# Kernel tuning notes

Hardware: AMD Instinct MI355X
Metric: run time of the kernel (lower is better)

Reference implementation:

```python
import jax, jax.numpy as jnp
import numpy as np

IN_FEATURES = 4096
OUT_FEATURES = 4096
GROUP_SIZE = 128


def _unpack_int4_last_dim(packed):
    # packed: [..., P] int32 -> [..., P*8] int32 nibbles in [0,15]
    shifts = jnp.arange(0, 32, 4, dtype=jnp.int32)
    u = (packed[..., None] >> shifts) & 15
    return u.reshape(*packed.shape[:-1], packed.shape[-1] * 8)


def setup_inputs() -> dict:
    key = jax.random.key(0)
    k1, k2, k3, k4, k5 = jax.random.split(key, 5)
    groups = IN_FEATURES // GROUP_SIZE  # 32
    x = jax.random.normal(k1, (4096, IN_FEATURES), dtype=jnp.float32)
    qweight = jax.random.randint(k2, (OUT_FEATURES, IN_FEATURES // 8), 0, 2147483647, dtype=jnp.int32)
    qzeros = jax.random.randint(k3, (OUT_FEATURES, groups // 8), 0, 2147483647, dtype=jnp.int32)
    scales = jax.random.uniform(k4, (OUT_FEATURES, groups), dtype=jnp.float32) * 0.02 + 0.001
    bias = jax.random.normal(k5, (OUT_FEATURES,), dtype=jnp.float32)
    return {"x": x, "qweight": qweight, "qzeros": qzeros, "scales": scales, "bias": bias}


def _dequantize_weight(qweight, qzeros, scales):
    # qweight: [out, in/8] -> w_int: [out, in]
    w_int = _unpack_int4_last_dim(qweight).astype(jnp.float32)
    # qzeros: [out, groups/8] -> zeros: [out, groups]
    zeros = _unpack_int4_last_dim(qzeros).astype(jnp.float32)
    group_ids = jnp.arange(IN_FEATURES) // GROUP_SIZE  # [in]
    # expand per-group scale/zero along in_features
    w = (w_int - zeros[:, group_ids]) * scales[:, group_ids]  # [out, in]
    return w


def reference(x, qweight, qzeros, scales, bias):
    w = _dequantize_weight(qweight, qzeros, scales)  # [out, in] fp32
    return x @ w.T + bias  # [tokens, out]
```

## Files before the change

### kernel.cpp

```cpp
#include <hip/hip_runtime.h>
#include <hip/hip_bf16.h>

#define TOKENS 4096
#define IN_F   4096
#define OUT_F  4096

typedef __bf16 bf16x8 __attribute__((ext_vector_type(8)));
typedef float  f32x4  __attribute__((ext_vector_type(4)));
typedef unsigned int u32;
typedef u32 u32x4 __attribute__((ext_vector_type(4)));

#define DEQ_BLOCKS 2048
#define CVT_BLOCKS 4096

__device__ __forceinline__ void gld_lds16(const void* g, void* l) {
    __builtin_amdgcn_global_load_lds(
        (const __attribute__((address_space(1))) u32*)g,
        (__attribute__((address_space(3))) u32*)l,
        16, 0, 0);
}

__global__ __launch_bounds__(256) void prep_kernel(
        const u32* __restrict__ qweight, const u32* __restrict__ qzeros,
        const float* __restrict__ scales, const float* __restrict__ x,
        __bf16* __restrict__ W, __bf16* __restrict__ A) {
    const int tid = threadIdx.x;
    if (blockIdx.x < DEQ_BLOCKS) {
        int idx4 = blockIdx.x * 256 + tid;
        int n  = idx4 >> 7;
        int p4 = (idx4 & 127) << 2;
        int g  = p4 >> 4;
        u32 qz = qzeros[(n << 2) + (g >> 3)];
        float z = (float)((qz >> ((g & 7) * 4)) & 15);
        float s = scales[(n << 5) + g];
        u32x4 qw = *(const u32x4*)(qweight + (size_t)n * 512 + p4);
        __bf16* dst = W + (size_t)n * IN_F + p4 * 8;
#pragma unroll
        for (int c = 0; c < 4; ++c) {
            bf16x8 h;
#pragma unroll
            for (int j = 0; j < 8; ++j) {
                float w = ((float)((qw[c] >> (4 * j)) & 15) - z) * s;
                h[j] = (__bf16)w;
            }
            *(bf16x8*)(dst + c * 8) = h;
        }
    } else {
        int idx = (blockIdx.x - DEQ_BLOCKS) * 256 + tid;
        const f32x4* xp = (const f32x4*)x + (size_t)idx * 4;
        f32x4 v0 = xp[0], v1 = xp[1], v2 = xp[2], v3 = xp[3];
        bf16x8 h0, h1;
#pragma unroll
        for (int j = 0; j < 4; ++j) {
            h0[j] = (__bf16)v0[j]; h0[4 + j] = (__bf16)v1[j];
            h1[j] = (__bf16)v2[j]; h1[4 + j] = (__bf16)v3[j];
        }
        bf16x8* ap = (bf16x8*)A + (size_t)idx * 2;
        ap[0] = h0; ap[1] = h1;
    }
}

__global__ __launch_bounds__(512, 2) void gemm8p(
        const __bf16* __restrict__ A, const __bf16* __restrict__ B,
        const float* __restrict__ bias, float* __restrict__ C) {
    __shared__ __align__(16) char lsA[65536];
    __shared__ __align__(16) char lsB[65536];

    const int t    = threadIdx.x;
    const int lane = t & 63, wave = t >> 6;
    const int lr   = lane & 15, quad = lane >> 4;
    const int wm   = (wave >> 2) * 128;
    const int wn   = (wave & 3) * 64;

    int bid = blockIdx.x;
    bid = (bid & 7) * 32 + (bid >> 3);
    const int bm = bid >> 4, bn = bid & 15;

    const __bf16* Abase = A + (size_t)bm * 256 * IN_F;
    const __bf16* Bbase = B + (size_t)bn * 256 * IN_F;

    const int srow0 = t >> 2;
    const int srow1 = 128 + (t >> 2);
    const int scol0 = ((t & 3) ^ ((srow0 >> 1) & 3)) * 8;
    const int scol1 = ((t & 3) ^ ((srow1 >> 1) & 3)) * 8;

#define STAGE(OPBASE, LS, KT, KH, BUF) do {                                  \
    int _kb = (((KT) & 63) * 64 + (KH) * 32);                                \
    gld_lds16(OPBASE + (size_t)srow0 * IN_F + _kb + scol0,                   \
              LS + ((BUF) * 2 + (KH)) * 16384 + t * 16);                     \
    gld_lds16(OPBASE + (size_t)srow1 * IN_F + _kb + scol1,                   \
              LS + ((BUF) * 2 + (KH)) * 16384 + 8192 + t * 16);              \
} while (0)

    const u32 slot16 = (u32)((quad ^ ((lr >> 1) & 3)) * 16);
    const u32 lsA0 = (u32)(size_t)(__attribute__((address_space(3))) char*)lsA;
    const u32 lsB0 = (u32)(size_t)(__attribute__((address_space(3))) char*)lsB;
    const u32 aA = lsA0 + (u32)((wm + lr) * 64) + slot16;
    const u32 aB = lsB0 + (u32)((wn + lr) * 64) + slot16;

    bf16x8 af0[4], af1[4], bf0[4], bf1[4];
    f32x4 acc[8][4] = {};

#define RA(BUF, KH) (((BUF) * 2 + (KH)) * 16384)
#define RB(BUF, KH) (((BUF) * 2 + (KH)) * 16384)

#define DSR(dst, base, OFF) do {                                             \
    u32x4 _r;                                                                \
    asm volatile("ds_read_b128 %0, %1 offset:%2"                             \
                 : "=v"(_r) : "v"(base), "n"(OFF));                          \
    dst = __builtin_bit_cast(bf16x8, _r);                                    \
} while (0)

#define G4(PM, I, AF, BF) do {                                               \
    _Pragma("unroll")                                                        \
    for (int j = 0; j < 4; ++j)                                              \
        acc[(PM) * 4 + (I)][j] = __builtin_amdgcn_mfma_f32_16x16x32_bf16(    \
            AF[(I)], BF[j], acc[(PM) * 4 + (I)][j], 0, 0, 0);                \
} while (0)

#define FENCE() asm volatile("" ::: "memory")
#define BAR()  do { FENCE(); __builtin_amdgcn_s_barrier(); FENCE(); } while (0)
#define VM6()  asm volatile("s_waitcnt vmcnt(6)" ::: "memory")
#define VM4()  asm volatile("s_waitcnt vmcnt(4)" ::: "memory")
#define PRIO(x) __builtin_amdgcn_s_setprio(x)
#define SB()   __builtin_amdgcn_sched_barrier(0)
#define LGKM0SB() do {                                                       \
    asm volatile("s_waitcnt lgkmcnt(0)" ::: "memory"); SB(); } while (0)

#define P0_BODY(KT, B) do {                                                  \
    STAGE(Abase, lsA, (KT) + 1, 1, 1 - (B));                                 \
    LGKM0SB(); PRIO(1);                                                      \
    G4(0,0,af0,bf0); SB(); DSR(af1[0], aA, RA(B,0)+4096+0*1024);             \
                           DSR(bf1[0], aB, RB(B,1)+0*1024); SB();            \
    G4(0,1,af0,bf0); SB(); DSR(af1[1], aA, RA(B,0)+4096+1*1024);             \
                           DSR(bf1[1], aB, RB(B,1)+1*1024); SB();            \
    G4(0,2,af0,bf0); SB(); DSR(af1[2], aA, RA(B,0)+4096+2*1024);             \
                           DSR(bf1[2], aB, RB(B,1)+2*1024); SB();            \
    G4(0,3,af0,bf0); SB(); DSR(af1[3], aA, RA(B,0)+4096+3*1024);             \
                           DSR(bf1[3], aB, RB(B,1)+3*1024); SB();            \
    PRIO(0); BAR();                                                          \
} while (0)

#define P1_BODY(KT, B) do {                                                  \
    STAGE(Bbase, lsB, (KT) + 1, 1, 1 - (B));                                 \
    LGKM0SB(); PRIO(1);                                                      \
    G4(1,0,af1,bf0); SB(); DSR(af0[0], aA, RA(B,1)+0*1024); SB();            \
    G4(1,1,af1,bf0); SB(); DSR(af0[1], aA, RA(B,1)+1*1024); SB();            \
    G4(1,2,af1,bf0); SB(); DSR(af0[2], aA, RA(B,1)+2*1024); SB();            \
    G4(1,3,af1,bf0); SB(); DSR(af0[3], aA, RA(B,1)+3*1024); SB();            \
    PRIO(0); BAR();                                                          \
} while (0)

#define P2_BODY(KT, B) do {                                                  \
    STAGE(Abase, lsA, (KT) + 2, 0, (B));                                     \
    VM6(); LGKM0SB(); PRIO(1);                                               \
    G4(0,0,af0,bf1); SB(); DSR(af1[0], aA, RA(B,1)+4096+0*1024);             \
                           DSR(bf0[0], aB, RB(1-(B),0)+0*1024); SB();        \
    G4(0,1,af0,bf1); SB(); DSR(af1[1], aA, RA(B,1)+4096+1*1024);             \
                           DSR(bf0[1], aB, RB(1-(B),0)+1*1024); SB();        \
    G4(0,2,af0,bf1); SB(); DSR(af1[2], aA, RA(B,1)+4096+2*1024);             \
                           DSR(bf0[2], aB, RB(1-(B),0)+2*1024); SB();        \
    G4(0,3,af0,bf1); SB(); DSR(af1[3], aA, RA(B,1)+4096+3*1024);             \
                           DSR(bf0[3], aB, RB(1-(B),0)+3*1024); SB();        \
    PRIO(0); BAR();                                                          \
} while (0)

#define P3_BODY(KT, B) do {                                                  \
    STAGE(Bbase, lsB, (KT) + 2, 0, (B));                                     \
    VM4(); LGKM0SB(); PRIO(1);                                               \
    G4(1,0,af1,bf1); SB(); DSR(af0[0], aA, RA(1-(B),0)+0*1024); SB();        \
    G4(1,1,af1,bf1); SB(); DSR(af0[1], aA, RA(1-(B),0)+1*1024); SB();        \
    G4(1,2,af1,bf1); SB(); DSR(af0[2], aA, RA(1-(B),0)+2*1024); SB();        \
    G4(1,3,af1,bf1); SB(); DSR(af0[3], aA, RA(1-(B),0)+3*1024); SB();        \
    PRIO(0); BAR();                                                          \
} while (0)

    STAGE(Abase, lsA, 0, 0, 0);
    STAGE(Bbase, lsB, 0, 0, 0);
    STAGE(Abase, lsA, 0, 1, 0);
    STAGE(Bbase, lsB, 0, 1, 0);
    STAGE(Abase, lsA, 1, 0, 1);
    STAGE(Bbase, lsB, 1, 0, 1);
    VM4();
    BAR();
    DSR(bf0[0], aB, RB(0,0)+0*1024); DSR(bf0[1], aB, RB(0,0)+1*1024);
    DSR(bf0[2], aB, RB(0,0)+2*1024); DSR(bf0[3], aB, RB(0,0)+3*1024);
    DSR(af0[0], aA, RA(0,0)+0*1024); DSR(af0[1], aA, RA(0,0)+1*1024);
    DSR(af0[2], aA, RA(0,0)+2*1024); DSR(af0[3], aA, RA(0,0)+3*1024);

    for (int kt = 0; kt < 64; kt += 2) {
        P0_BODY(kt, 0); P1_BODY(kt, 0); P2_BODY(kt, 0); P3_BODY(kt, 0);
        P0_BODY(kt + 1, 1); P1_BODY(kt + 1, 1);
        P2_BODY(kt + 1, 1); P3_BODY(kt + 1, 1);
    }

    asm volatile("s_waitcnt vmcnt(0) lgkmcnt(0)" ::: "memory");

    const int row0 = bm * 256 + wm + quad * 4;
    const int col0 = bn * 256 + wn + lr;
#pragma unroll
    for (int j = 0; j < 4; ++j) {
        const int col = col0 + j * 16;
        const float bv = bias[col];
#pragma unroll
        for (int i = 0; i < 8; ++i) {
            const int row = row0 + i * 16;
#pragma unroll
            for (int r = 0; r < 4; ++r)
                C[(size_t)(row + r) * OUT_F + col] = acc[i][j][r] + bv;
        }
    }
}

extern "C" void kernel_launch(void* const* d_in, const int* in_sizes, int n_in,
                              void* d_out, int out_size, void* d_ws, size_t ws_size,
                              hipStream_t stream) {
    (void)in_sizes; (void)n_in; (void)out_size; (void)ws_size;
    const float* x       = (const float*)d_in[0];
    const u32*   qweight = (const u32*)d_in[1];
    const u32*   qzeros  = (const u32*)d_in[2];
    const float* scales  = (const float*)d_in[3];
    const float* bias    = (const float*)d_in[4];
    float* out = (float*)d_out;

    __bf16* W   = (__bf16*)d_ws;
    __bf16* Abf = (__bf16*)((char*)d_ws + (size_t)OUT_F * IN_F * 2);

    prep_kernel<<<dim3(DEQ_BLOCKS + CVT_BLOCKS), dim3(256), 0, stream>>>(
        qweight, qzeros, scales, x, W, Abf);
    gemm8p<<<dim3(256), dim3(512), 0, stream>>>(Abf, W, bias, out);
}
```

Measured before the change: 246.4 us.

## Restructure GEMM main loop into two barrier phases and coalesce prep accesses

The GEMM inner loop goes from four barrier-separated phases per K-half to two. Each phase now issues both A and B staging loads and 32 MFMAs, interleaved with LDS fragment reads. Halving the barriers and waitcnt points should cut sync overhead, at the cost of more fragment registers (six bf16x8 arrays) and possible occupancy or spill pressure. The prep kernel also switches to strided per-thread indexing so dequant and convert loads/stores coalesce across lanes, trading 16-byte vector loads for narrower ones.

```diff
diff --git a/kernel.cpp b/kernel.cpp
--- a/kernel.cpp
+++ b/kernel.cpp
@@ -6,6 +6,7 @@
 #define OUT_F  4096
 
 typedef __bf16 bf16x8 __attribute__((ext_vector_type(8)));
+typedef __bf16 bf16x4 __attribute__((ext_vector_type(4)));
 typedef float  f32x4  __attribute__((ext_vector_type(4)));
 typedef unsigned int u32;
 typedef u32 u32x4 __attribute__((ext_vector_type(4)));
@@ -26,41 +27,43 @@
         __bf16* __restrict__ W, __bf16* __restrict__ A) {
     const int tid = threadIdx.x;
     if (blockIdx.x < DEQ_BLOCKS) {
-        int idx4 = blockIdx.x * 256 + tid;
-        int n  = idx4 >> 7;
-        int p4 = (idx4 & 127) << 2;
-        int g  = p4 >> 4;
-        u32 qz = qzeros[(n << 2) + (g >> 3)];
-        float z = (float)((qz >> ((g & 7) * 4)) & 15);
-        float s = scales[(n << 5) + g];
-        u32x4 qw = *(const u32x4*)(qweight + (size_t)n * 512 + p4);
-        __bf16* dst = W + (size_t)n * IN_F + p4 * 8;
+        int idx = blockIdx.x * 256 + tid;
+        int n = idx >> 7;
+        int T = idx & 127;
+        const u32* qwrow = qweight + (size_t)n * 512;
+        __bf16* dst = W + (size_t)n * IN_F;
 #pragma unroll
         for (int c = 0; c < 4; ++c) {
+            int p = T + c * 128;
+            int g = p >> 4;
+            u32 qz = qzeros[(n << 2) + c];
+            float z = (float)((qz >> ((g & 7) * 4)) & 15);
+            float s = scales[(n << 5) + g];
+            u32 qw = qwrow[p];
             bf16x8 h;
 #pragma unroll
             for (int j = 0; j < 8; ++j) {
-                float w = ((float)((qw[c] >> (4 * j)) & 15) - z) * s;
+                float w = ((float)((qw >> (4 * j)) & 15) - z) * s;
                 h[j] = (__bf16)w;
             }
-            *(bf16x8*)(dst + c * 8) = h;
+            *(bf16x8*)(dst + p * 8) = h;
         }
     } else {
-        int idx = (blockIdx.x - DEQ_BLOCKS) * 256 + tid;
-        const f32x4* xp = (const f32x4*)x + (size_t)idx * 4;
-        f32x4 v0 = xp[0], v1 = xp[1], v2 = xp[2], v3 = xp[3];
-        bf16x8 h0, h1;
-#pragma unroll
-        for (int j = 0; j < 4; ++j) {
-            h0[j] = (__bf16)v0[j]; h0[4 + j] = (__bf16)v1[j];
-            h1[j] = (__bf16)v2[j]; h1[4 + j] = (__bf16)v3[j];
+        int b = blockIdx.x - DEQ_BLOCKS;
+        int base = b * 4096 + tid * 4;
+#pragma unroll
+        for (int k = 0; k < 4; ++k) {
+            int f = base + k * 1024;
+            f32x4 v = *(const f32x4*)(x + f);
+            bf16x4 h;
+            h[0] = (__bf16)v[0]; h[1] = (__bf16)v[1];
+            h[2] = (__bf16)v[2]; h[3] = (__bf16)v[3];
+            *(bf16x4*)(A + f) = h;
         }
-        bf16x8* ap = (bf16x8*)A + (size_t)idx * 2;
-        ap[0] = h0; ap[1] = h1;
     }
 }
 
-__global__ __launch_bounds__(512, 2) void gemm8p(
+__global__ __launch_bounds__(512, 2) void gemm2p(
         const __bf16* __restrict__ A, const __bf16* __restrict__ B,
         const float* __restrict__ bias, float* __restrict__ C) {
     __shared__ __align__(16) char lsA[65536];
@@ -98,7 +101,8 @@
     const u32 aA = lsA0 + (u32)((wm + lr) * 64) + slot16;
     const u32 aB = lsB0 + (u32)((wn + lr) * 64) + slot16;
 
-    bf16x8 af0[4], af1[4], bf0[4], bf1[4];
+    bf16x8 afP0[4], afP1[4], bfE[4];
+    bf16x8 afN0[4], afN1[4], bfO[4];
     f32x4 acc[8][4] = {};
 
 #define RA(BUF, KH) (((BUF) * 2 + (KH)) * 16384)
@@ -120,59 +124,52 @@
 
 #define FENCE() asm volatile("" ::: "memory")
 #define BAR()  do { FENCE(); __builtin_amdgcn_s_barrier(); FENCE(); } while (0)
-#define VM6()  asm volatile("s_waitcnt vmcnt(6)" ::: "memory")
 #define VM4()  asm volatile("s_waitcnt vmcnt(4)" ::: "memory")
 #define PRIO(x) __builtin_amdgcn_s_setprio(x)
 #define SB()   __builtin_amdgcn_sched_barrier(0)
 #define LGKM0SB() do {                                                       \
     asm volatile("s_waitcnt lgkmcnt(0)" ::: "memory"); SB(); } while (0)
 
-#define P0_BODY(KT, B) do {                                                  \
+#define PHA(KT, B) do {                                                      \
     STAGE(Abase, lsA, (KT) + 1, 1, 1 - (B));                                 \
-    LGKM0SB(); PRIO(1);                                                      \
-    G4(0,0,af0,bf0); SB(); DSR(af1[0], aA, RA(B,0)+4096+0*1024);             \
-                           DSR(bf1[0], aB, RB(B,1)+0*1024); SB();            \
-    G4(0,1,af0,bf0); SB(); DSR(af1[1], aA, RA(B,0)+4096+1*1024);             \
-                           DSR(bf1[1], aB, RB(B,1)+1*1024); SB();            \
-    G4(0,2,af0,bf0); SB(); DSR(af1[2], aA, RA(B,0)+4096+2*1024);             \
-                           DSR(bf1[2], aB, RB(B,1)+2*1024); SB();            \
-    G4(0,3,af0,bf0); SB(); DSR(af1[3], aA, RA(B,0)+4096+3*1024);             \
-                           DSR(bf1[3], aB, RB(B,1)+3*1024); SB();            \
-    PRIO(0); BAR();                                                          \
-} while (0)
-
-#define P1_BODY(KT, B) do {                                                  \
     STAGE(Bbase, lsB, (KT) + 1, 1, 1 - (B));                                 \
     LGKM0SB(); PRIO(1);                                                      \
-    G4(1,0,af1,bf0); SB(); DSR(af0[0], aA, RA(B,1)+0*1024); SB();            \
-    G4(1,1,af1,bf0); SB(); DSR(af0[1], aA, RA(B,1)+1*1024); SB();            \
-    G4(1,2,af1,bf0); SB(); DSR(af0[2], aA, RA(B,1)+2*1024); SB();            \
-    G4(1,3,af1,bf0); SB(); DSR(af0[3], aA, RA(B,1)+3*1024); SB();            \
-    PRIO(0); BAR();                                                          \
-} while (0)
-
-#define P2_BODY(KT, B) do {                                                  \
+    G4(0,0,afP0,bfE); SB(); DSR(afN0[0], aA, RA(B,1)+0*1024);                \
+                            DSR(afN1[0], aA, RA(B,1)+4096+0*1024); SB();     \
+    G4(0,1,afP0,bfE); SB(); DSR(afN0[1], aA, RA(B,1)+1*1024);                \
+                            DSR(afN1[1], aA, RA(B,1)+4096+1*1024); SB();     \
+    G4(0,2,afP0,bfE); SB(); DSR(afN0[2], aA, RA(B,1)+2*1024);                \
+                            DSR(afN1[2], aA, RA(B,1)+4096+2*1024); SB();     \
+    G4(0,3,afP0,bfE); SB(); DSR(afN0[3], aA, RA(B,1)+3*1024);                \
+                            DSR(afN1[3], aA, RA(B,1)+4096+3*1024); SB();     \
+    G4(1,0,afP1,bfE); SB(); DSR(bfO[0], aB, RB(B,1)+0*1024);                 \
+                            DSR(bfO[1], aB, RB(B,1)+1*1024); SB();           \
+    G4(1,1,afP1,bfE); SB(); DSR(bfO[2], aB, RB(B,1)+2*1024);                 \
+                            DSR(bfO[3], aB, RB(B,1)+3*1024); SB();           \
+    G4(1,2,afP1,bfE);                                                        \
+    G4(1,3,afP1,bfE);                                                        \
+    PRIO(0); VM4(); BAR();                                                   \
+} while (0)
+
+#define PHB(KT, B) do {                                                      \
     STAGE(Abase, lsA, (KT) + 2, 0, (B));                                     \
-    VM6(); LGKM0SB(); PRIO(1);                                               \
-    G4(0,0,af0,bf1); SB(); DSR(af1[0], aA, RA(B,1)+4096+0*1024);             \
-                           DSR(bf0[0], aB, RB(1-(B),0)+0*1024); SB();        \
-    G4(0,1,af0,bf1); SB(); DSR(af1[1], aA, RA(B,1)+4096+1*1024);             \
-                           DSR(bf0[1], aB, RB(1-(B),0)+1*1024); SB();        \
-    G4(0,2,af0,bf1); SB(); DSR(af1[2], aA, RA(B,1)+4096+2*1024);             \
-                           DSR(bf0[2], aB, RB(1-(B),0)+2*1024); SB();        \
-    G4(0,3,af0,bf1); SB(); DSR(af1[3], aA, RA(B,1)+4096+3*1024);             \
-                           DSR(bf0[3], aB, RB(1-(B),0)+3*1024); SB();        \
-    PRIO(0); BAR();                                                          \
-} while (0)
-
-#define P3_BODY(KT, B) do {                                                  \
     STAGE(Bbase, lsB, (KT) + 2, 0, (B));                                     \
-    VM4(); LGKM0SB(); PRIO(1);                                               \
-    G4(1,0,af1,bf1); SB(); DSR(af0[0], aA, RA(1-(B),0)+0*1024); SB();        \
-    G4(1,1,af1,bf1); SB(); DSR(af0[1], aA, RA(1-(B),0)+1*1024); SB();        \
-    G4(1,2,af1,bf1); SB(); DSR(af0[2], aA, RA(1-(B),0)+2*1024); SB();        \
-    G4(1,3,af1,bf1); SB(); DSR(af0[3], aA, RA(1-(B),0)+3*1024); SB();        \
-    PRIO(0); BAR();                                                          \
+    LGKM0SB(); PRIO(1);                                                      \
+    G4(0,0,afN0,bfO); SB(); DSR(afP0[0], aA, RA(1-(B),0)+0*1024);            \
+                            DSR(afP1[0], aA, RA(1-(B),0)+4096+0*1024); SB(); \
+    G4(0,1,afN0,bfO); SB(); DSR(afP0[1], aA, RA(1-(B),0)+1*1024);            \
+                            DSR(afP1[1], aA, RA(1-(B),0)+4096+1*1024); SB(); \
+    G4(0,2,afN0,bfO); SB(); DSR(afP0[2], aA, RA(1-(B),0)+2*1024);            \
+                            DSR(afP1[2], aA, RA(1-(B),0)+4096+2*1024); SB(); \
+    G4(0,3,afN0,bfO); SB(); DSR(afP0[3], aA, RA(1-(B),0)+3*1024);            \
+                            DSR(afP1[3], aA, RA(1-(B),0)+4096+3*1024); SB(); \
+    G4(1,0,afN1,bfO); SB(); DSR(bfE[0], aB, RB(1-(B),0)+0*1024);             \
+                            DSR(bfE[1], aB, RB(1-(B),0)+1*1024); SB();       \
+    G4(1,1,afN1,bfO); SB(); DSR(bfE[2], aB, RB(1-(B),0)+2*1024);             \
+                            DSR(bfE[3], aB, RB(1-(B),0)+3*1024); SB();       \
+    G4(1,2,afN1,bfO);                                                        \
+    G4(1,3,afN1,bfO);                                                        \
+    PRIO(0); VM4(); BAR();                                                   \
 } while (0)
 
     STAGE(Abase, lsA, 0, 0, 0);
@@ -183,15 +180,16 @@
     STAGE(Bbase, lsB, 1, 0, 1);
     VM4();
     BAR();
-    DSR(bf0[0], aB, RB(0,0)+0*1024); DSR(bf0[1], aB, RB(0,0)+1*1024);
-    DSR(bf0[2], aB, RB(0,0)+2*1024); DSR(bf0[3], aB, RB(0,0)+3*1024);
-    DSR(af0[0], aA, RA(0,0)+0*1024); DSR(af0[1], aA, RA(0,0)+1*1024);
-    DSR(af0[2], aA, RA(0,0)+2*1024); DSR(af0[3], aA, RA(0,0)+3*1024);
+    DSR(bfE[0], aB, RB(0,0)+0*1024); DSR(bfE[1], aB, RB(0,0)+1*1024);
+    DSR(bfE[2], aB, RB(0,0)+2*1024); DSR(bfE[3], aB, RB(0,0)+3*1024);
+    DSR(afP0[0], aA, RA(0,0)+0*1024); DSR(afP0[1], aA, RA(0,0)+1*1024);
+    DSR(afP0[2], aA, RA(0,0)+2*1024); DSR(afP0[3], aA, RA(0,0)+3*1024);
+    DSR(afP1[0], aA, RA(0,0)+4096+0*1024); DSR(afP1[1], aA, RA(0,0)+4096+1*1024);
+    DSR(afP1[2], aA, RA(0,0)+4096+2*1024); DSR(afP1[3], aA, RA(0,0)+4096+3*1024);
 
     for (int kt = 0; kt < 64; kt += 2) {
-        P0_BODY(kt, 0); P1_BODY(kt, 0); P2_BODY(kt, 0); P3_BODY(kt, 0);
-        P0_BODY(kt + 1, 1); P1_BODY(kt + 1, 1);
-        P2_BODY(kt + 1, 1); P3_BODY(kt + 1, 1);
+        PHA(kt, 0); PHB(kt, 0);
+        PHA(kt + 1, 1); PHB(kt + 1, 1);
     }
 
     asm volatile("s_waitcnt vmcnt(0) lgkmcnt(0)" ::: "memory");
@@ -228,5 +226,5 @@
 
     prep_kernel<<<dim3(DEQ_BLOCKS + CVT_BLOCKS), dim3(256), 0, stream>>>(
         qweight, qzeros, scales, x, W, Abf);
-    gemm8p<<<dim3(256), dim3(512), 0, stream>>>(Abf, W, bias, out);
-}
+    gemm2p<<<dim3(256), dim3(512), 0, stream>>>(Abf, W, bias, out);
+}
```

Result: faster. 241.5 us (-2.0%).
